# Kernel optimization log

Measured on AMD Instinct MI355X. Metric: run time of the kernel, lower is better.

The kernel has to match this reference:

```python
import jax, jax.numpy as jnp
import numpy as np
from jax import lax

DN = ('NCHW', 'OIHW', 'NCHW')

def conv(x, w, b, stride=1):
    y = lax.conv_general_dilated(x, w, window_strides=(stride, stride),
                                 padding='VALID', dimension_numbers=DN)
    return y + b[None, :, None, None]

def maxpool(x, k=3, s=2):
    return lax.reduce_window(x, -jnp.inf, lax.max,
                             (1, 1, k, k), (1, 1, s, s), 'VALID')

def setup_inputs() -> dict:
    key = jax.random.key(0)
    ks = jax.random.split(key, 7)
    B = 2048
    x = jax.random.normal(ks[0], (B, 1, 28, 28), dtype=jnp.float32)
    w1 = jax.random.normal(ks[1], (64, 1, 3, 3), dtype=jnp.float32)
    b1 = jax.random.normal(ks[2], (64,), dtype=jnp.float32)
    w2 = jax.random.normal(ks[3], (64, 64, 3, 3), dtype=jnp.float32)
    b2 = jax.random.normal(ks[4], (64,), dtype=jnp.float32)
    w3 = jax.random.normal(ks[5], (10, 64, 4, 4), dtype=jnp.float32)
    b3 = jax.random.normal(ks[6], (10,), dtype=jnp.float32)
    return {"x": x, "w1": w1, "b1": b1, "w2": w2, "b2": b2, "w3": w3, "b3": b3}

def reference(x, w1, b1, w2, b2, w3, b3):
    h = conv(x, w1, b1)            # [B,64,26,26]
    h = maxpool(h)                 # [B,64,12,12]
    h = jnp.maximum(h, 0.0)
    h = conv(h, w2, b2)            # [B,64,10,10]
    h = maxpool(h)                 # [B,64,4,4]
    h = jnp.maximum(h, 0.0)
    h = conv(h, w3, b3)            # [B,10,1,1]
    return h.reshape(h.shape[0], -1)  # [B,10]
```

## Files before the change

kernel.cpp:

```cpp
#include <hip/hip_runtime.h>


typedef __attribute__((ext_vector_type(8))) short short8;
typedef __attribute__((ext_vector_type(4))) float f32x4;

__device__ inline short f2bf(float f) {
    union { float f; unsigned u; } v; v.f = f;
    unsigned r = (v.u + 0x7FFFu + ((v.u >> 16) & 1u)) >> 16;
    return (short)r;
}

__global__ __launch_bounds__(256) void prep_w2(const float* __restrict__ w2,
                                               short* __restrict__ w2r) {
    int i = blockIdx.x * 256 + threadIdx.x;
    if (i >= 36864) return;
    int s = i >> 12, cout = (i >> 6) & 63, cin = i & 63;
    w2r[i] = f2bf(w2[cout * 576 + cin * 9 + s]);
}

__global__ __launch_bounds__(256) void convnet_fused(
    const float* __restrict__ x,
    const float* __restrict__ w1,
    const float* __restrict__ b1,
    const short* __restrict__ w2r,
    const float* __restrict__ b2,
    const float* __restrict__ w3,
    const float* __restrict__ b3,
    float* __restrict__ out)
{
    __shared__ float lds_f[7424];
    short* h1t  = (short*)lds_f;
    float* img  = lds_f + 5184;
    float* cbuf = lds_f;
    float* h2t  = lds_f + 6400;
    float* prt  = lds_f;

    const int n_img = blockIdx.x;
    const int t = threadIdx.x;
    const int c = t >> 2;
    const int q = t & 3;

    const float* img_g = x + (size_t)n_img * 784;
    for (int i = t; i < 784; i += 256) img[i] = img_g[i];
    __syncthreads();

    {
        const int oy = (q >> 1) * 6, ox = (q & 1) * 6;
        const int iy0 = 2 * oy, ix0 = 2 * ox;
        float w[9];
        #pragma unroll
        for (int k = 0; k < 9; ++k) w[k] = w1[c * 9 + k];
        const float bias = b1[c];

        float in0[15], in1[15], in2[15];
        #pragma unroll
        for (int s = 0; s < 15; ++s) in0[s] = img[(iy0 + 0) * 28 + ix0 + s];
        #pragma unroll
        for (int s = 0; s < 15; ++s) in1[s] = img[(iy0 + 1) * 28 + ix0 + s];
        float cm[3][6];

        #pragma unroll
        for (int r = 0; r < 13; ++r) {
            #pragma unroll
            for (int s = 0; s < 15; ++s) in2[s] = img[(iy0 + r + 2) * 28 + ix0 + s];
            #pragma unroll
            for (int px = 0; px < 6; ++px) cm[r % 3][px] = -1e30f;
            #pragma unroll
            for (int xx = 0; xx < 13; ++xx) {
                float a = bias;
                #pragma unroll
                for (int j = 0; j < 3; ++j) {
                    a += in0[xx + j] * w[j];
                    a += in1[xx + j] * w[3 + j];
                    a += in2[xx + j] * w[6 + j];
                }
                if ((xx & 1) == 0) {
                    if (xx >= 2 && xx <= 12) cm[r % 3][xx / 2 - 1] = fmaxf(cm[r % 3][xx / 2 - 1], a);
                    if (xx <= 10)            cm[r % 3][xx / 2]     = fmaxf(cm[r % 3][xx / 2], a);
                } else {
                    cm[r % 3][xx / 2] = fmaxf(cm[r % 3][xx / 2], a);
                }
            }
            if (r >= 2 && (r & 1) == 0) {
                const int py = r / 2 - 1;
                #pragma unroll
                for (int px = 0; px < 6; ++px) {
                    float m = fmaxf(fmaxf(cm[0][px], cm[1][px]), cm[2][px]);
                    h1t[((oy + py) * 12 + ox + px) * 72 + c] = f2bf(fmaxf(m, 0.0f));
                }
            }
            #pragma unroll
            for (int s = 0; s < 15; ++s) { in0[s] = in1[s]; in1[s] = in2[s]; }
        }
    }
    __syncthreads();

    const int wv = t >> 6, lane = t & 63;
    const int quad = lane >> 4, mrow = lane & 15;
    {
        int base_el[7];
        #pragma unroll
        for (int nt = 0; nt < 7; ++nt) {
            int n = nt * 16 + mrow; if (n > 99) n = 99;
            int y = n / 10, xx = n - y * 10;
            base_el[nt] = (y * 12 + xx) * 72;
        }
        f32x4 acc[7];
        #pragma unroll
        for (int nt = 0; nt < 7; ++nt) acc[nt] = (f32x4){0.f, 0.f, 0.f, 0.f};

        #pragma unroll
        for (int ks = 0; ks < 18; ++ks) {
            const int s = ks >> 1, h = ks & 1;
            const int ky = s / 3, kx = s - ky * 3;
            const short8 a = *(const short8*)(w2r + s * 4096 + (wv * 16 + mrow) * 64
                                              + h * 32 + quad * 8);
            #pragma unroll
            for (int nt = 0; nt < 7; ++nt) {
                const short8 b = *(const short8*)(h1t + base_el[nt]
                                                  + (ky * 12 + kx) * 72 + h * 32 + quad * 8);
                acc[nt] = __builtin_amdgcn_mfma_f32_16x16x32_bf16(a, b, acc[nt], 0, 0, 0);
            }
        }
        __syncthreads();
        #pragma unroll
        for (int nt = 0; nt < 7; ++nt) {
            const int n = nt * 16 + mrow;
            if (n < 100) {
                #pragma unroll
                for (int r = 0; r < 4; ++r) {
                    const int cout = wv * 16 + quad * 4 + r;
                    cbuf[cout * 100 + n] = acc[nt][r] + b2[cout];
                }
            }
        }
    }
    __syncthreads();

    {
        const float* cb = cbuf + c * 100;
        #pragma unroll
        for (int k = 0; k < 4; ++k) {
            const int pos = q * 4 + k;
            const int py = pos >> 2, px = pos & 3;
            float m = -1e30f;
            #pragma unroll
            for (int a = 0; a < 3; ++a)
                #pragma unroll
                for (int b = 0; b < 3; ++b)
                    m = fmaxf(m, cb[(2 * py + a) * 10 + (2 * px + b)]);
            h2t[pos * 64 + c] = fmaxf(m, 0.0f);
        }
    }
    __syncthreads();

    if (t < 160) {
        const int o = t >> 4, l = t & 15;
        const float* w3o = w3 + o * 1024;
        float s = 0.0f;
        #pragma unroll
        for (int cc = 0; cc < 4; ++cc) {
            const int cin = l * 4 + cc;
            const float4 wv4a = *(const float4*)(w3o + cin * 16);
            const float4 wv4b = *(const float4*)(w3o + cin * 16 + 4);
            const float4 wv4c = *(const float4*)(w3o + cin * 16 + 8);
            const float4 wv4d = *(const float4*)(w3o + cin * 16 + 12);
            const float* hh = h2t + cin;
            s += hh[0*64] * wv4a.x + hh[1*64] * wv4a.y + hh[2*64] * wv4a.z + hh[3*64] * wv4a.w;
            s += hh[4*64] * wv4b.x + hh[5*64] * wv4b.y + hh[6*64] * wv4b.z + hh[7*64] * wv4b.w;
            s += hh[8*64] * wv4c.x + hh[9*64] * wv4c.y + hh[10*64] * wv4c.z + hh[11*64] * wv4c.w;
            s += hh[12*64] * wv4d.x + hh[13*64] * wv4d.y + hh[14*64] * wv4d.z + hh[15*64] * wv4d.w;
        }
        prt[t] = s;
    }
    __syncthreads();
    if (t < 10) {
        float s = b3[t];
        #pragma unroll
        for (int l = 0; l < 16; ++l) s += prt[t * 16 + l];
        out[(size_t)n_img * 10 + t] = s;
    }
}

extern "C" void kernel_launch(void* const* d_in, const int* in_sizes, int n_in,
                              void* d_out, int out_size, void* d_ws, size_t ws_size,
                              hipStream_t stream) {
    const float* x  = (const float*)d_in[0];
    const float* w1 = (const float*)d_in[1];
    const float* b1 = (const float*)d_in[2];
    const float* w2 = (const float*)d_in[3];
    const float* b2 = (const float*)d_in[4];
    const float* w3 = (const float*)d_in[5];
    const float* b3 = (const float*)d_in[6];
    float* out = (float*)d_out;
    short* w2r = (short*)d_ws;

    const int B = in_sizes[0] / 784;
    prep_w2<<<144, 256, 0, stream>>>(w2, w2r);
    convnet_fused<<<B, 256, 0, stream>>>(x, w1, b1, w2r, b2, w3, b3, out);
}
```

Before: 112.0 us.

## Fuse w2 bf16 conversion into main kernel and vectorize conv1 LDS row loads

Drops the separate prep_w2 launch. Each wave now reads its fp32 w2 rows directly with float4 loads and converts them to bf16 fragments in registers before the MFMA loop. Conv1 input rows are loaded from LDS as float4 into a rotating three-row register buffer, replacing scalar loads and register shifts. The cost is redundant w2 conversion in every block (2048 blocks) plus higher register pressure from holding nine A fragments, in exchange for one fewer kernel launch and cheaper conv1 loads.

```diff
diff --git a/kernel.cpp b/kernel.cpp
--- a/kernel.cpp
+++ b/kernel.cpp
@@ -10,19 +10,11 @@
     return (short)r;
 }
 
-__global__ __launch_bounds__(256) void prep_w2(const float* __restrict__ w2,
-                                               short* __restrict__ w2r) {
-    int i = blockIdx.x * 256 + threadIdx.x;
-    if (i >= 36864) return;
-    int s = i >> 12, cout = (i >> 6) & 63, cin = i & 63;
-    w2r[i] = f2bf(w2[cout * 576 + cin * 9 + s]);
-}
-
 __global__ __launch_bounds__(256) void convnet_fused(
     const float* __restrict__ x,
     const float* __restrict__ w1,
     const float* __restrict__ b1,
-    const short* __restrict__ w2r,
+    const float* __restrict__ w2,
     const float* __restrict__ b2,
     const float* __restrict__ w3,
     const float* __restrict__ b3,
@@ -52,17 +44,30 @@
         for (int k = 0; k < 9; ++k) w[k] = w1[c * 9 + k];
         const float bias = b1[c];
 
-        float in0[15], in1[15], in2[15];
-        #pragma unroll
-        for (int s = 0; s < 15; ++s) in0[s] = img[(iy0 + 0) * 28 + ix0 + s];
-        #pragma unroll
-        for (int s = 0; s < 15; ++s) in1[s] = img[(iy0 + 1) * 28 + ix0 + s];
+        float rows[3][16];
+        {
+            const float* s0 = img + iy0 * 28 + ix0;
+            const float* s1 = img + (iy0 + 1) * 28 + ix0;
+            #pragma unroll
+            for (int m = 0; m < 4; ++m) {
+                *(float4*)(rows[0] + 4 * m) = *(const float4*)(s0 + 4 * m);
+                *(float4*)(rows[1] + 4 * m) = *(const float4*)(s1 + 4 * m);
+            }
+        }
         float cm[3][6];
 
         #pragma unroll
         for (int r = 0; r < 13; ++r) {
-            #pragma unroll
-            for (int s = 0; s < 15; ++s) in2[s] = img[(iy0 + r + 2) * 28 + ix0 + s];
+            {
+                const float* s2 = img + (iy0 + r + 2) * 28 + ix0;
+                float* dst = rows[(r + 2) % 3];
+                #pragma unroll
+                for (int m = 0; m < 4; ++m)
+                    *(float4*)(dst + 4 * m) = *(const float4*)(s2 + 4 * m);
+            }
+            const float* r0 = rows[r % 3];
+            const float* r1 = rows[(r + 1) % 3];
+            const float* r2 = rows[(r + 2) % 3];
             #pragma unroll
             for (int px = 0; px < 6; ++px) cm[r % 3][px] = -1e30f;
             #pragma unroll
@@ -70,9 +75,9 @@
                 float a = bias;
                 #pragma unroll
                 for (int j = 0; j < 3; ++j) {
-                    a += in0[xx + j] * w[j];
-                    a += in1[xx + j] * w[3 + j];
-                    a += in2[xx + j] * w[6 + j];
+                    a += r0[xx + j] * w[j];
+                    a += r1[xx + j] * w[3 + j];
+                    a += r2[xx + j] * w[6 + j];
                 }
                 if ((xx & 1) == 0) {
                     if (xx >= 2 && xx <= 12) cm[r % 3][xx / 2 - 1] = fmaxf(cm[r % 3][xx / 2 - 1], a);
@@ -89,8 +94,6 @@
                     h1t[((oy + py) * 12 + ox + px) * 72 + c] = f2bf(fmaxf(m, 0.0f));
                 }
             }
-            #pragma unroll
-            for (int s = 0; s < 15; ++s) { in0[s] = in1[s]; in1[s] = in2[s]; }
         }
     }
     __syncthreads();
@@ -109,17 +112,30 @@
         #pragma unroll
         for (int nt = 0; nt < 7; ++nt) acc[nt] = (f32x4){0.f, 0.f, 0.f, 0.f};
 
-        #pragma unroll
-        for (int ks = 0; ks < 18; ++ks) {
-            const int s = ks >> 1, h = ks & 1;
-            const int ky = s / 3, kx = s - ky * 3;
-            const short8 a = *(const short8*)(w2r + s * 4096 + (wv * 16 + mrow) * 64
-                                              + h * 32 + quad * 8);
-            #pragma unroll
-            for (int nt = 0; nt < 7; ++nt) {
-                const short8 b = *(const short8*)(h1t + base_el[nt]
-                                                  + (ky * 12 + kx) * 72 + h * 32 + quad * 8);
-                acc[nt] = __builtin_amdgcn_mfma_f32_16x16x32_bf16(a, b, acc[nt], 0, 0, 0);
+        const int cout = wv * 16 + mrow;
+        #pragma unroll
+        for (int h = 0; h < 2; ++h) {
+            const int c0 = h * 32 + quad * 8;
+            const float* runp = w2 + cout * 576 + c0 * 9;
+            short8 af[9];
+            #pragma unroll
+            for (int m = 0; m < 18; ++m) {
+                const float4 v = *(const float4*)(runp + 4 * m);
+                const int i0 = 4 * m;
+                af[(i0 + 0) % 9][(i0 + 0) / 9] = f2bf(v.x);
+                af[(i0 + 1) % 9][(i0 + 1) / 9] = f2bf(v.y);
+                af[(i0 + 2) % 9][(i0 + 2) / 9] = f2bf(v.z);
+                af[(i0 + 3) % 9][(i0 + 3) / 9] = f2bf(v.w);
+            }
+            #pragma unroll
+            for (int s = 0; s < 9; ++s) {
+                const int ky = s / 3, kx = s - ky * 3;
+                const int boff = (ky * 12 + kx) * 72 + h * 32 + quad * 8;
+                #pragma unroll
+                for (int nt = 0; nt < 7; ++nt) {
+                    const short8 b = *(const short8*)(h1t + base_el[nt] + boff);
+                    acc[nt] = __builtin_amdgcn_mfma_f32_16x16x32_bf16(af[s], b, acc[nt], 0, 0, 0);
+                }
             }
         }
         __syncthreads();
@@ -129,8 +145,8 @@
             if (n < 100) {
                 #pragma unroll
                 for (int r = 0; r < 4; ++r) {
-                    const int cout = wv * 16 + quad * 4 + r;
-                    cbuf[cout * 100 + n] = acc[nt][r] + b2[cout];
+                    const int co = wv * 16 + quad * 4 + r;
+                    cbuf[co * 100 + n] = acc[nt][r] + b2[co];
                 }
             }
         }
@@ -193,9 +209,7 @@
     const float* w3 = (const float*)d_in[5];
     const float* b3 = (const float*)d_in[6];
     float* out = (float*)d_out;
-    short* w2r = (short*)d_ws;
 
     const int B = in_sizes[0] / 784;
-    prep_w2<<<144, 256, 0, stream>>>(w2, w2r);
-    convnet_fused<<<B, 256, 0, stream>>>(x, w1, b1, w2r, b2, w3, b3, out);
+    convnet_fused<<<B, 256, 0, stream>>>(x, w1, b1, w2, b2, w3, b3, out);
 }
```

Measured after the change: 135.8 us. 1.21x slower.
